# Performance work log

Measured on AMD Instinct MI355X. Metric: run time of the kernel, lower is better.

## Reference

```python
import jax, jax.numpy as jnp
import numpy as np
from jax import lax

EPS = 0.1  # regularization_strength, 'kl' regularization (torchsort.soft_rank)


@jax.jit
def _pav_kl(s, logw):
    """Batched pool-adjacent-violators for KL-regularized isotonic regression.
    s: [B, n] (rows sorted descending), logw: [n] = log([n, n-1, ..., 1]).
    Port of torchsort's isotonic_kl kernel; the sequential algorithm is
    flattened so each while-loop iteration performs one step per row.
    Returns (sol [B,n] block-constant dual solution, block_id [B,n])."""
    B, n = s.shape
    rows = jnp.arange(B)
    w = jnp.broadcast_to(logw, (B, n))

    def g(A, idx):  # batched gather with clipped index
        return A[rows, jnp.clip(idx, 0, n - 1)]

    def cond(st):
        return jnp.any(st[0] < n)

    def body(st):
        i, k, sol_prev, merging, target, lse_y, lse_w, sol = st
        active = i < n
        scan_mode = active & ~merging
        k_nm = g(target, i) + 1
        at_end = k_nm >= n
        decreasing = g(sol, i) > g(sol, k_nm)
        advance = scan_mode & (at_end | decreasing)
        start_merge = scan_mode & ~at_end & ~decreasing

        # one merge step for rows currently merging: pool block at i with block at k
        ly = jnp.logaddexp(g(lse_y, i), g(lse_y, k))
        lw = jnp.logaddexp(g(lse_w, i), g(lse_w, k))
        k_next = g(target, k) + 1
        stop = merging & ((k_next >= n) | (sol_prev > g(sol, k_next)))

        wi = jnp.where(merging, i, 0)  # inactive rows write back old value
        lse_y = lse_y.at[rows, wi].set(jnp.where(merging, ly, lse_y[rows, wi]))
        lse_w = lse_w.at[rows, wi].set(jnp.where(merging, lw, lse_w[rows, wi]))
        sol = sol.at[rows, wi].set(jnp.where(merging, ly - lw, sol[rows, wi]))

        p1 = jnp.where(stop, i, 0)
        target = target.at[rows, p1].set(jnp.where(stop, k_next - 1, target[rows, p1]))
        p2 = jnp.where(stop, jnp.clip(k_next - 1, 0, n - 1), 0)
        target = target.at[rows, p2].set(jnp.where(stop, i, target[rows, p2]))

        i_back = jnp.where(i > 0, g(target, i - 1), i)  # pool with preceding block
        i_new = jnp.where(advance, k_nm, jnp.where(stop, i_back, i))
        k_new = jnp.where(start_merge, k_nm, jnp.where(merging & ~stop, k_next, k))
        merging_new = (merging & ~stop) | start_merge
        sol_prev_new = jnp.where(start_merge, g(sol, i), sol_prev)
        return (i_new, k_new, sol_prev_new, merging_new, target, lse_y, lse_w, sol)

    init = (jnp.zeros(B, jnp.int32), jnp.zeros(B, jnp.int32),
            jnp.zeros(B, s.dtype), jnp.zeros(B, bool),
            jnp.broadcast_to(jnp.arange(n, dtype=jnp.int32), (B, n)).copy(),
            s, w, s - w)
    _, _, _, _, target, _, _, sol = lax.while_loop(cond, body, init)

    # reconstruct block-constant solution and per-position block ids
    def recon(carry, xs):
        block_end, val, bid = carry
        j, sol_j, tgt_j = xs
        newb = j > block_end
        val = jnp.where(newb, sol_j, val)
        block_end = jnp.where(newb, tgt_j, block_end)
        bid = bid + newb.astype(jnp.int32)
        return (block_end, val, bid), (val, bid)

    carry0 = (jnp.full(B, -1, jnp.int32), sol[:, 0], jnp.full(B, -1, jnp.int32))
    _, (sol_full, block_id) = lax.scan(
        recon, carry0, (jnp.arange(n, dtype=jnp.int32), sol.T, target.T))
    return sol_full.T, block_id.T


def _soft_rank_core(x):
    # x: [B, n] -> soft ranks [B, n]  (torchsort.soft_rank, 'kl')
    B, n = x.shape
    theta = x / EPS
    perm = jnp.argsort(-theta, axis=-1)  # stable descending sort
    s = jnp.take_along_axis(theta, perm, axis=-1)
    logw = jnp.log(jnp.arange(n, 0, -1).astype(x.dtype))  # log([n..1])
    sol, block_id = _pav_kl(s, logw)
    r_sorted = jnp.exp(s - sol)  # = softmax(s_block) * sum(w_block)
    inv = jnp.argsort(perm, axis=-1)
    ranks = jnp.take_along_axis(r_sorted, inv, axis=-1)
    return ranks, (r_sorted, inv, perm, block_id)


def soft_rank_kl(x):
    return _soft_rank_core(x)[0]


def setup_inputs() -> dict:
    key = jax.random.key(0)
    k1, k2 = jax.random.split(key)
    x1 = jax.random.normal(k1, (16, 256, 2048), dtype=jnp.float32)
    x2 = jax.random.normal(k2, (16, 256, 2048), dtype=jnp.float32)
    return {"x1": x1, "x2": x2}


def reference(x1, x2):
    S, T, V = x1.shape  # n_sents, trg_length, scored dim
    r1 = soft_rank_kl(x1.reshape(-1, V))
    r2 = soft_rank_kl(x2.reshape(-1, V))
    c1 = r1 - jnp.mean(r1, axis=-1, keepdims=True)
    c2 = r2 - jnp.mean(r2, axis=-1, keepdims=True)
    corr = jnp.sum(c1 * c2, axis=-1) / (
        jnp.linalg.norm(c1, axis=-1) * jnp.linalg.norm(c2, axis=-1))
    return (1.0 - corr).reshape(S, T)
```

## Files before the change

kernel.cpp:

```cpp
#include <hip/hip_runtime.h>
#include <math.h>

#define N   2048
#define NT  256
#define V   8

__device__ __forceinline__ int wsum(int h, int e) {
    return (((N - h) + (N - e)) * (e - h + 1)) >> 1;
}

__device__ __forceinline__ int pidx(int j) { return j + (j >> 5); }

__device__ __forceinline__ unsigned desc_key(float t) {
    unsigned u = __float_as_uint(t);
    unsigned a = (u & 0x80000000u) ? ~u : (u ^ 0x80000000u);
    return ~a;
}
__device__ __forceinline__ float decode_key(unsigned d) {
    unsigned a = ~d;
    unsigned u = (a & 0x80000000u) ? (a ^ 0x80000000u) : ~a;
    return __uint_as_float(u);
}

__device__ __forceinline__ unsigned qkey(float t, int j) {
    return ((desc_key(t) + 0x400u) & 0xFFFFF800u) | (unsigned)j;
}

#define INVALID_P 0xFFFFFFFFu
__device__ __forceinline__ unsigned packYH(float Y, int h) {
    return ((__float_as_uint(Y) + 0x400u) & 0xFFFFF800u) | (unsigned)h;
}
__device__ __forceinline__ float upY(unsigned u) { return __uint_as_float(u & 0xFFFFF800u); }
__device__ __forceinline__ int   upH(unsigned u) { return (int)(u & 0x7FFu); }

__device__ __forceinline__ void ceu(unsigned &a, unsigned &b, bool up) {
    unsigned mn = (a < b) ? a : b;
    unsigned mx = (a < b) ? b : a;
    a = up ? mn : mx;
    b = up ? mx : mn;
}

__device__ __forceinline__ void cea(unsigned &a, unsigned &b) {
    unsigned mn = (a < b) ? a : b;
    unsigned mx = (a < b) ? b : a;
    a = mn; b = mx;
}

__device__ __forceinline__ void merge8a(unsigned* r) {
    cea(r[0], r[4]); cea(r[1], r[5]); cea(r[2], r[6]); cea(r[3], r[7]);
    cea(r[0], r[2]); cea(r[1], r[3]); cea(r[4], r[6]); cea(r[5], r[7]);
    cea(r[0], r[1]); cea(r[2], r[3]); cea(r[4], r[5]); cea(r[6], r[7]);
}

__device__ __forceinline__ void shfl_ce(unsigned* r, int d, bool keepMin) {
    #pragma unroll
    for (int q = 0; q < V; ++q) {
        unsigned p = __shfl_xor(r[q], d, 64);
        bool lt = r[q] < p;
        r[q] = (lt == keepMin) ? r[q] : p;
    }
}

__device__ __forceinline__ int next_head_p(const unsigned* sU,
                                           const unsigned char* sBeg,
                                           const unsigned char* sEnd,
                                           int lane, int d, int bEnd)
{
    if (d + 1 < (int)sEnd[lane]) return upH(sU[(d + 1) * NT + lane]);
    for (int l = lane + 1; l < bEnd; ++l)
        if (sBeg[l] != sEnd[l]) return upH(sU[(int)sBeg[l] * NT + l]);
    return bEnd << 3;
}

__global__ void __launch_bounds__(NT, 6)
fused_kernel(const float* __restrict__ x1, const float* __restrict__ x2,
             float* __restrict__ out)
{
    __shared__ unsigned       s_kx[N + (N >> 5)];
    __shared__ unsigned       s_u [N + (N >> 5)];
    __shared__ unsigned short s_inv[N];
    __shared__ unsigned char  sBeg[NT], sEnd[NT];
    __shared__ float          s_red[NT / 64][5];
    __shared__ unsigned       swF[NT / 64];
    __shared__ int            swB[NT / 64];

    float* s_kxf = (float*)s_kx;

    const int p    = blockIdx.x;
    const int tid  = threadIdx.x;
    const int lane = tid & 63;
    const int wid  = tid >> 6;

    float S1 = 0.f, Q1 = 0.f, S2 = 0.f, Q2 = 0.f, P = 0.f;
    float rv1[V];

    for (int ph = 0; ph < 2; ++ph) {
        const float* __restrict__ x = ph ? x2 : x1;
        const size_t base = (size_t)p * N;

        const float4* __restrict__ xv = (const float4*)(x + base + tid * V);
        float4 a0 = xv[0], a1 = xv[1];
        const int bse = tid * V;
        unsigned r[V];
        r[0] = qkey(a0.x * 10.0f, bse + 0); r[1] = qkey(a0.y * 10.0f, bse + 1);
        r[2] = qkey(a0.z * 10.0f, bse + 2); r[3] = qkey(a0.w * 10.0f, bse + 3);
        r[4] = qkey(a1.x * 10.0f, bse + 4); r[5] = qkey(a1.y * 10.0f, bse + 5);
        r[6] = qkey(a1.z * 10.0f, bse + 6); r[7] = qkey(a1.w * 10.0f, bse + 7);

        ceu(r[0], r[1], true);  ceu(r[2], r[3], false);
        ceu(r[4], r[5], true);  ceu(r[6], r[7], false);
        ceu(r[0], r[2], true);  ceu(r[1], r[3], true);
        ceu(r[4], r[6], false); ceu(r[5], r[7], false);
        ceu(r[0], r[1], true);  ceu(r[2], r[3], true);
        ceu(r[4], r[5], false); ceu(r[6], r[7], false);

        unsigned m = ((tid & 1) == 0) ? 0u : 0xFFFFFFFFu;
        #pragma unroll
        for (int q = 0; q < V; ++q) r[q] ^= m;
        merge8a(r);

        #pragma unroll
        for (int kk = 4; kk <= 11; ++kk) {
            const unsigned mn_ = ((tid & (1 << (kk - 3))) == 0) ? 0u : 0xFFFFFFFFu;
            const unsigned dm = m ^ mn_;
            m = mn_;
            #pragma unroll
            for (int q = 0; q < V; ++q) r[q] ^= dm;
            #pragma unroll
            for (int jb = kk - 1; jb >= 3; --jb) {
                const int d = 1 << (jb - 3);
                if (d >= 64) {
                    __syncthreads();
                    #pragma unroll
                    for (int q = 0; q < V; ++q) s_kx[pidx(tid * V + q)] = r[q];
                    __syncthreads();
                    const bool keepMin = ((tid & d) == 0);
                    const int ptid = tid ^ d;
                    #pragma unroll
                    for (int q = 0; q < V; ++q) {
                        unsigned pv = s_kx[pidx(ptid * V + q)];
                        bool lt = r[q] < pv;
                        r[q] = (lt == keepMin) ? r[q] : pv;
                    }
                } else {
                    shfl_ce(r, d, (tid & d) == 0);
                }
            }
            merge8a(r);
        }

        __syncthreads();

        {
            float4 c0 = xv[0], c1 = xv[1];
            s_kx[pidx(bse + 0)] = desc_key(c0.x * 10.0f);
            s_kx[pidx(bse + 1)] = desc_key(c0.y * 10.0f);
            s_kx[pidx(bse + 2)] = desc_key(c0.z * 10.0f);
            s_kx[pidx(bse + 3)] = desc_key(c0.w * 10.0f);
            s_kx[pidx(bse + 4)] = desc_key(c1.x * 10.0f);
            s_kx[pidx(bse + 5)] = desc_key(c1.y * 10.0f);
            s_kx[pidx(bse + 6)] = desc_key(c1.z * 10.0f);
            s_kx[pidx(bse + 7)] = desc_key(c1.w * 10.0f);
        }
        __syncthreads();

        {
            unsigned fkv[V];
            #pragma unroll
            for (int k = 0; k < V; ++k) {
                const int idx = (int)(r[k] & 0x7FFu);
                fkv[k] = s_kx[pidx(idx)];
                s_inv[idx] = (unsigned short)(bse + k);
            }
            float eY[V];
            #pragma unroll
            for (int k = 0; k < V; ++k) eY[k] = __expf(decode_key(fkv[k]));

            int   sp = 0;
            float t0Y = 0.f, t1Y = 0.f;
            int   t0h = 0,   t1h = 0;
            #pragma unroll
            for (int k = 0; k < V; ++k) {
                const int j = bse + k;
                float cY = eY[k];
                int   ch = j;
                while (sp > 0) {
                    float cW = (float)wsum(ch, j);
                    float tW = (float)wsum(t0h, ch - 1);
                    if (t0Y * cW > cY * tW) break;
                    cY += t0Y; ch = t0h;
                    --sp;
                    t0Y = t1Y; t0h = t1h;
                    if (sp > 1) {
                        unsigned u = s_u[(sp - 2) * NT + tid];
                        t1Y = upY(u); t1h = upH(u);
                    }
                }
                s_u[sp * NT + tid] = packYH(cY, ch);
                t1Y = t0Y; t1h = t0h;
                t0Y = cY;  t0h = ch;
                ++sp;
            }
            sBeg[tid] = 0; sEnd[tid] = (unsigned char)sp;
        }
        __syncthreads();

        for (int lev = 0; lev < 8; ++lev) {
            const int g = 1 << lev;
            if ((tid & (2 * g - 1)) == 0) {
                const int a = tid, mid = tid + g, b = tid + 2 * g;
                int l0 = mid - 1;
                while (l0 >= a && sBeg[l0] == sEnd[l0]) --l0;
                int l1 = mid;
                while (l1 < b && sBeg[l1] == sEnd[l1]) ++l1;
                if (l0 >= a && l1 < b) {
                    int d0 = (int)sEnd[l0] - 1;
                    unsigned tu = s_u[d0 * NT + l0];
                    float tY = upY(tu); int th_ = upH(tu);
                    int te = (mid << 3) - 1;
                    int d1 = (int)sBeg[l1];
                    unsigned cu = s_u[d1 * NT + l1];
                    float cY = upY(cu); int ch = upH(cu);
                    int ce = next_head_p(s_u, sBeg, sEnd, l1, d1, b) - 1;
                    if (!(tY * (float)wsum(ch, ce) > cY * (float)wsum(th_, te))) {
                        sBeg[l1] = (unsigned char)(d1 + 1);
                        for (;;) {
                            if (l0 >= a &&
                                !(tY * (float)wsum(ch, ce) > cY * (float)wsum(th_, te))) {
                                cY += tY; ch = th_;
                                sEnd[l0] = (unsigned char)((int)sEnd[l0] - 1);
                                if (sBeg[l0] == sEnd[l0]) {
                                    do { --l0; } while (l0 >= a && sBeg[l0] == sEnd[l0]);
                                }
                                if (l0 >= a) {
                                    int dd = (int)sEnd[l0] - 1;
                                    unsigned uu = s_u[dd * NT + l0];
                                    tY = upY(uu); te = th_ - 1; th_ = upH(uu);
                                }
                                continue;
                            }
                            while (l1 < b && sBeg[l1] == sEnd[l1]) ++l1;
                            if (l1 < b) {
                                int dn = (int)sBeg[l1];
                                unsigned nu = s_u[dn * NT + l1];
                                float nY = upY(nu); int nh = upH(nu);
                                int ne = next_head_p(s_u, sBeg, sEnd, l1, dn, b) - 1;
                                if (!(cY * (float)wsum(nh, ne) > nY * (float)wsum(ch, ce))) {
                                    cY += nY; ce = ne;
                                    sBeg[l1] = (unsigned char)(dn + 1);
                                    continue;
                                }
                            }
                            break;
                        }
                        int lh = ch >> 3;
                        if (ch >= (mid << 3)) {
                            int nb = (int)sBeg[lh] - 1;
                            sBeg[lh] = (unsigned char)nb;
                            s_u[nb * NT + lh] = packYH(cY, ch);
                        } else {
                            int nb2 = (int)sEnd[lh];
                            s_u[nb2 * NT + lh] = packYH(cY, ch);
                            sEnd[lh] = (unsigned char)(nb2 + 1);
                        }
                    }
                }
            }
            __syncthreads();
        }

        const int b0 = sBeg[tid], b1 = sEnd[tid];
        unsigned myLast  = (b1 > b0) ? s_u[(b1 - 1) * NT + tid] : INVALID_P;
        int      myFirst = (b1 > b0) ? upH(s_u[b0 * NT + tid]) : N;

        unsigned fv = myLast;
        #pragma unroll
        for (int off = 1; off < 64; off <<= 1) {
            unsigned o = (unsigned)__shfl_up((int)fv, off);
            if (fv == INVALID_P) fv = o;
        }
        unsigned cF = (unsigned)__shfl_up((int)fv, 1);
        if (lane == 0) cF = INVALID_P;
        int bv = myFirst;
        #pragma unroll
        for (int off = 1; off < 64; off <<= 1) {
            int o = __shfl_down(bv, off);
            if (bv == N) bv = o;
        }
        int cB = __shfl_down(bv, 1);
        if (lane == 63) cB = N;
        if (lane == 63) swF[wid] = fv;
        if (lane == 0)  swB[wid] = bv;
        __syncthreads();
        if (cF == INVALID_P)
            for (int w = wid - 1; w >= 0; --w)
                if (swF[w] != INVALID_P) { cF = swF[w]; break; }
        if (cB == N)
            for (int w = wid + 1; w < NT / 64; ++w)
                if (swB[w] != N) { cB = swB[w]; break; }

        {
            int dptr = b0;
            int nxtOwn = (dptr < b1) ? upH(s_u[dptr * NT + tid]) : N;
            unsigned cur = cF;
            #pragma unroll
            for (int q = 0; q < V; ++q) {
                int j = bse + q;
                if (j == nxtOwn) {
                    cur = s_u[dptr * NT + tid];
                    ++dptr;
                    nxtOwn = (dptr < b1) ? upH(s_u[dptr * NT + tid]) : N;
                }
                s_kx[pidx(j)] = cur;
            }
        }
        {
            int dptr2 = b1 - 1;
            int h2 = (dptr2 >= b0) ? upH(s_u[dptr2 * NT + tid]) : -1;
            int nxt = cB;
            #pragma unroll
            for (int q = V - 1; q >= 0; --q) {
                int j = bse + q;
                int e = nxt - 1;
                unsigned cu = s_kx[pidx(j)];
                s_kxf[pidx(j)] = (float)wsum(upH(cu), e) / upY(cu);
                if (j == h2) {
                    nxt = j; --dptr2;
                    h2 = (dptr2 >= b0) ? upH(s_u[dptr2 * NT + tid]) : -1;
                }
            }
        }
        __syncthreads();

        {
            float4 c0 = xv[0], c1 = xv[1];
            float xx[V] = {c0.x, c0.y, c0.z, c0.w, c1.x, c1.y, c1.z, c1.w};
            #pragma unroll
            for (int q = 0; q < V; ++q) {
                int jq = (int)s_inv[bse + q];
                float rv = __expf(xx[q] * 10.0f) * s_kxf[pidx(jq)];
                if (ph == 0) {
                    rv1[q] = rv;
                    S1 += rv; Q1 += rv * rv;
                } else {
                    S2 += rv; Q2 += rv * rv; P += rv1[q] * rv;
                }
            }
        }
        __syncthreads();
    }

    #pragma unroll
    for (int off = 32; off > 0; off >>= 1) {
        S1 += __shfl_down(S1, off);
        Q1 += __shfl_down(Q1, off);
        S2 += __shfl_down(S2, off);
        Q2 += __shfl_down(Q2, off);
        P  += __shfl_down(P,  off);
    }
    if (lane == 0) {
        s_red[wid][0] = S1; s_red[wid][1] = Q1; s_red[wid][2] = S2;
        s_red[wid][3] = Q2; s_red[wid][4] = P;
    }
    __syncthreads();
    if (tid == 0) {
        for (int w = 1; w < NT / 64; ++w) {
            S1 += s_red[w][0]; Q1 += s_red[w][1]; S2 += s_red[w][2];
            Q2 += s_red[w][3]; P  += s_red[w][4];
        }
        const float inv_n = 1.0f / (float)N;
        float num = P  - S1 * S2 * inv_n;
        float d1  = Q1 - S1 * S1 * inv_n;
        float d2  = Q2 - S2 * S2 * inv_n;
        out[p] = 1.0f - num / sqrtf(d1 * d2);
    }
}

extern "C" void kernel_launch(void* const* d_in, const int* in_sizes, int n_in,
                              void* d_out, int out_size, void* d_ws, size_t ws_size,
                              hipStream_t stream) {
    const float* x1 = (const float*)d_in[0];
    const float* x2 = (const float*)d_in[1];
    float* out = (float*)d_out;
    const int nrows = in_sizes[0] / N;
    fused_kernel<<<nrows, NT, 0, stream>>>(x1, x2, out);
}
```

Before: 270.3 us.

## Track non-empty lane stacks with occupancy bitmask for upper merge levels

```diff
diff --git a/kernel.cpp b/kernel.cpp
--- a/kernel.cpp
+++ b/kernel.cpp
@@ -22,9 +22,6 @@
     return __uint_as_float(u);
 }
 
-__device__ __forceinline__ unsigned qkey(float t, int j) {
-    return ((desc_key(t) + 0x400u) & 0xFFFFF800u) | (unsigned)j;
-}
 
 #define INVALID_P 0xFFFFFFFFu
 __device__ __forceinline__ unsigned packYH(float Y, int h) {
@@ -61,15 +58,39 @@
     }
 }
 
-__device__ __forceinline__ int next_head_p(const unsigned* sU,
-                                           const unsigned char* sBeg,
-                                           const unsigned char* sEnd,
-                                           int lane, int d, int bEnd)
+__device__ __forceinline__ int nsb(const unsigned long long* occ, int l, int b) {
+    if (l >= b) return b;
+    int w = l >> 6;
+    const int wb = b >> 6;
+    unsigned long long mm = occ[w] & (~0ULL << (l & 63));
+    while (mm == 0) { if (++w >= wb) return b; mm = occ[w]; }
+    return (w << 6) + (int)__ffsll(mm) - 1;
+}
+__device__ __forceinline__ int psb(const unsigned long long* occ, int l, int a) {
+    if (l < a) return a - 1;
+    int w = l >> 6;
+    const int wa = a >> 6;
+    unsigned long long mm = occ[w] & (~0ULL >> (63 - (l & 63)));
+    while (mm == 0) { if (--w < wa) return a - 1; mm = occ[w]; }
+    return (w << 6) + 63 - (int)__clzll(mm);
+}
+
+__device__ __forceinline__ int next_head2(const unsigned* sU,
+                                          const unsigned char* sBeg,
+                                          const unsigned char* sEnd,
+                                          const unsigned long long* occ,
+                                          bool useOcc,
+                                          int lane_, int d, int bEnd)
 {
-    if (d + 1 < (int)sEnd[lane]) return upH(sU[(d + 1) * NT + lane]);
-    for (int l = lane + 1; l < bEnd; ++l)
-        if (sBeg[l] != sEnd[l]) return upH(sU[(int)sBeg[l] * NT + l]);
-    return bEnd << 3;
+    if (d + 1 < (int)sEnd[lane_]) return upH(sU[(d + 1) * NT + lane_]);
+    int l2;
+    if (useOcc) {
+        l2 = nsb(occ, lane_ + 1, bEnd);
+    } else {
+        l2 = lane_ + 1;
+        while (l2 < bEnd && sBeg[l2] == sEnd[l2]) ++l2;
+    }
+    return (l2 < bEnd) ? upH(sU[(int)sBeg[l2] * NT + l2]) : (bEnd << 3);
 }
 
 __global__ void __launch_bounds__(NT, 6)
@@ -80,6 +101,7 @@
     __shared__ unsigned       s_u [N + (N >> 5)];
     __shared__ unsigned short s_inv[N];
     __shared__ unsigned char  sBeg[NT], sEnd[NT];
+    __shared__ unsigned long long s_occ[NT / 64];
     __shared__ float          s_red[NT / 64][5];
     __shared__ unsigned       swF[NT / 64];
     __shared__ int            swB[NT / 64];
@@ -101,11 +123,17 @@
         const float4* __restrict__ xv = (const float4*)(x + base + tid * V);
         float4 a0 = xv[0], a1 = xv[1];
         const int bse = tid * V;
+        unsigned dk[V];
+        dk[0] = desc_key(a0.x * 10.0f); dk[1] = desc_key(a0.y * 10.0f);
+        dk[2] = desc_key(a0.z * 10.0f); dk[3] = desc_key(a0.w * 10.0f);
+        dk[4] = desc_key(a1.x * 10.0f); dk[5] = desc_key(a1.y * 10.0f);
+        dk[6] = desc_key(a1.z * 10.0f); dk[7] = desc_key(a1.w * 10.0f);
         unsigned r[V];
-        r[0] = qkey(a0.x * 10.0f, bse + 0); r[1] = qkey(a0.y * 10.0f, bse + 1);
-        r[2] = qkey(a0.z * 10.0f, bse + 2); r[3] = qkey(a0.w * 10.0f, bse + 3);
-        r[4] = qkey(a1.x * 10.0f, bse + 4); r[5] = qkey(a1.y * 10.0f, bse + 5);
-        r[6] = qkey(a1.z * 10.0f, bse + 6); r[7] = qkey(a1.w * 10.0f, bse + 7);
+        #pragma unroll
+        for (int q = 0; q < V; ++q) {
+            s_kx[pidx(bse + q)] = dk[q];
+            r[q] = ((dk[q] + 0x400u) & 0xFFFFF800u) | (unsigned)(bse + q);
+        }
 
         ceu(r[0], r[1], true);  ceu(r[2], r[3], false);
         ceu(r[4], r[5], true);  ceu(r[6], r[7], false);
@@ -132,13 +160,13 @@
                 if (d >= 64) {
                     __syncthreads();
                     #pragma unroll
-                    for (int q = 0; q < V; ++q) s_kx[pidx(tid * V + q)] = r[q];
+                    for (int q = 0; q < V; ++q) s_u[pidx(tid * V + q)] = r[q];
                     __syncthreads();
                     const bool keepMin = ((tid & d) == 0);
                     const int ptid = tid ^ d;
                     #pragma unroll
                     for (int q = 0; q < V; ++q) {
-                        unsigned pv = s_kx[pidx(ptid * V + q)];
+                        unsigned pv = s_u[pidx(ptid * V + q)];
                         bool lt = r[q] < pv;
                         r[q] = (lt == keepMin) ? r[q] : pv;
                     }
@@ -149,19 +177,6 @@
             merge8a(r);
         }
 
-        __syncthreads();
-
-        {
-            float4 c0 = xv[0], c1 = xv[1];
-            s_kx[pidx(bse + 0)] = desc_key(c0.x * 10.0f);
-            s_kx[pidx(bse + 1)] = desc_key(c0.y * 10.0f);
-            s_kx[pidx(bse + 2)] = desc_key(c0.z * 10.0f);
-            s_kx[pidx(bse + 3)] = desc_key(c0.w * 10.0f);
-            s_kx[pidx(bse + 4)] = desc_key(c1.x * 10.0f);
-            s_kx[pidx(bse + 5)] = desc_key(c1.y * 10.0f);
-            s_kx[pidx(bse + 6)] = desc_key(c1.z * 10.0f);
-            s_kx[pidx(bse + 7)] = desc_key(c1.w * 10.0f);
-        }
         __syncthreads();
 
         {
@@ -207,12 +222,23 @@
 
         for (int lev = 0; lev < 8; ++lev) {
             const int g = 1 << lev;
+            const bool useOcc = (lev >= 5);
+            if (lev == 5) {
+                unsigned long long ob = __ballot(sBeg[tid] != sEnd[tid]);
+                if (lane == 0) s_occ[wid] = ob;
+            }
             if ((tid & (2 * g - 1)) == 0) {
                 const int a = tid, mid = tid + g, b = tid + 2 * g;
-                int l0 = mid - 1;
-                while (l0 >= a && sBeg[l0] == sEnd[l0]) --l0;
-                int l1 = mid;
-                while (l1 < b && sBeg[l1] == sEnd[l1]) ++l1;
+                int l0, l1;
+                if (useOcc) {
+                    l0 = psb(s_occ, mid - 1, a);
+                    l1 = nsb(s_occ, mid, b);
+                } else {
+                    l0 = mid - 1;
+                    while (l0 >= a && sBeg[l0] == sEnd[l0]) --l0;
+                    l1 = mid;
+                    while (l1 < b && sBeg[l1] == sEnd[l1]) ++l1;
+                }
                 if (l0 >= a && l1 < b) {
                     int d0 = (int)sEnd[l0] - 1;
                     unsigned tu = s_u[d0 * NT + l0];
@@ -221,16 +247,23 @@
                     int d1 = (int)sBeg[l1];
                     unsigned cu = s_u[d1 * NT + l1];
                     float cY = upY(cu); int ch = upH(cu);
-                    int ce = next_head_p(s_u, sBeg, sEnd, l1, d1, b) - 1;
+                    int ce = next_head2(s_u, sBeg, sEnd, s_occ, useOcc, l1, d1, b) - 1;
                     if (!(tY * (float)wsum(ch, ce) > cY * (float)wsum(th_, te))) {
                         sBeg[l1] = (unsigned char)(d1 + 1);
+                        if (useOcc && sBeg[l1] == sEnd[l1])
+                            s_occ[l1 >> 6] &= ~(1ULL << (l1 & 63));
                         for (;;) {
                             if (l0 >= a &&
                                 !(tY * (float)wsum(ch, ce) > cY * (float)wsum(th_, te))) {
                                 cY += tY; ch = th_;
                                 sEnd[l0] = (unsigned char)((int)sEnd[l0] - 1);
                                 if (sBeg[l0] == sEnd[l0]) {
-                                    do { --l0; } while (l0 >= a && sBeg[l0] == sEnd[l0]);
+                                    if (useOcc) {
+                                        s_occ[l0 >> 6] &= ~(1ULL << (l0 & 63));
+                                        l0 = psb(s_occ, l0 - 1, a);
+                                    } else {
+                                        do { --l0; } while (l0 >= a && sBeg[l0] == sEnd[l0]);
+                                    }
                                 }
                                 if (l0 >= a) {
                                     int dd = (int)sEnd[l0] - 1;
@@ -239,15 +272,21 @@
                                 }
                                 continue;
                             }
-                            while (l1 < b && sBeg[l1] == sEnd[l1]) ++l1;
+                            if (useOcc) {
+                                l1 = nsb(s_occ, l1, b);
+                            } else {
+                                while (l1 < b && sBeg[l1] == sEnd[l1]) ++l1;
+                            }
                             if (l1 < b) {
                                 int dn = (int)sBeg[l1];
                                 unsigned nu = s_u[dn * NT + l1];
                                 float nY = upY(nu); int nh = upH(nu);
-                                int ne = next_head_p(s_u, sBeg, sEnd, l1, dn, b) - 1;
+                                int ne = next_head2(s_u, sBeg, sEnd, s_occ, useOcc, l1, dn, b) - 1;
                                 if (!(cY * (float)wsum(nh, ne) > nY * (float)wsum(ch, ce))) {
                                     cY += nY; ce = ne;
                                     sBeg[l1] = (unsigned char)(dn + 1);
+                                    if (useOcc && sBeg[l1] == sEnd[l1])
+                                        s_occ[l1 >> 6] &= ~(1ULL << (l1 & 63));
                                     continue;
                                 }
                             }
@@ -263,6 +302,8 @@
                             s_u[nb2 * NT + lh] = packYH(cY, ch);
                             sEnd[lh] = (unsigned char)(nb2 + 1);
                         }
+                        if (useOcc)
+                            s_occ[lh >> 6] |= (1ULL << (lh & 63));
                     }
                 }
             }
```

Result: slower. 277.6 us (+2.7%).
